# Performance work log

Hardware: AMD Instinct MI355X
Metric: run time of the kernel (lower is better)

Reference implementation:

```python
import jax, jax.numpy as jnp
import numpy as np

N = 50000; R2 = 200; D = 200; E = 200000; B = 1024
NB = 4; NF = 96; KS = 7; KW = 10; KH = 20
FLAT = (2 * KW - KS + 1) * (KH - KS + 1) * NF  # 18816
EPS = 1e-5


def _bn2d(x, g, b):
    # BatchNorm2d over NCHW with batch statistics
    m = x.mean(axis=(0, 2, 3), keepdims=True)
    v = x.var(axis=(0, 2, 3), keepdims=True)
    return (x - m) * jax.lax.rsqrt(v + EPS) * g[None, :, None, None] + b[None, :, None, None]


def _bn1d(x, g, b):
    m = x.mean(axis=0, keepdims=True)
    v = x.var(axis=0, keepdims=True)
    return (x - m) * jax.lax.rsqrt(v + EPS) * g[None, :] + b[None, :]


def setup_inputs() -> dict:
    key = jax.random.key(0)
    ks = jax.random.split(key, 16)
    s = 0.05
    return {
        'ent_emb': jax.random.normal(ks[0], (N, D)) * s,
        'rel_table': jax.random.normal(ks[1], (R2, D)) * s,
        'basis': jax.random.normal(ks[2], (NB, D, D)) * s,
        'att': jax.random.normal(ks[3], (R2, NB)) * s,
        'root': jax.random.normal(ks[4], (D, D)) * s,
        'gbias': jnp.zeros((D,), jnp.float32),
        'bn0_g': jnp.ones((1,), jnp.float32), 'bn0_b': jnp.zeros((1,), jnp.float32),
        'conv_k': jax.random.normal(ks[5], (NF, 1, KS, KS)) * s,
        'conv_b': jnp.zeros((NF,), jnp.float32),
        'bn1_g': jnp.ones((NF,), jnp.float32), 'bn1_b': jnp.zeros((NF,), jnp.float32),
        'fc_W': jax.random.normal(ks[6], (FLAT, D)) * s,
        'fc_b': jnp.zeros((D,), jnp.float32),
        'bn2_g': jnp.ones((D,), jnp.float32), 'bn2_b': jnp.zeros((D,), jnp.float32),
        'ent_bias': jnp.zeros((N,), jnp.float32),
        'edge_norm': jax.random.uniform(ks[7], (E,)),
        'entity': jnp.arange(N, dtype=jnp.int32),
        'edge_index': jax.random.randint(ks[8], (2, E), 0, N, dtype=jnp.int32),
        'edge_type': jax.random.randint(ks[9], (E,), 0, R2, dtype=jnp.int32),
        'src': jax.random.randint(ks[10], (B,), 0, N, dtype=jnp.int32),
        'rel': jax.random.randint(ks[11], (B,), 0, R2, dtype=jnp.int32),
    }


def reference(ent_emb, rel_table, basis, att, root, gbias, bn0_g, bn0_b,
              conv_k, conv_b, bn1_g, bn1_b, fc_W, fc_b, bn2_g, bn2_b,
              ent_bias, edge_norm, entity, edge_index, edge_type, src, rel):
    # --- MGCNConv: relational message passing ---
    x = ent_emb[entity]                                  # [N, D]
    xj = x[edge_index[0]]                                # gather source nodes [E, D]
    # basis-decomposed per-edge transform: msg_e = x_j @ (att[r_e] . basis)
    xb = jnp.einsum('ei,bio->ebo', xj, basis)            # [E, NB, D]
    msg = jnp.einsum('eb,ebo->eo', att[edge_type], xb)   # [E, D]
    msg = msg * edge_norm[:, None]
    aggr = jax.ops.segment_sum(msg, edge_index[1], num_segments=N)  # scatter-add [N, D]
    h = aggr + x @ root + gbias[None, :]                 # update (root + bias)

    # --- ConvE decoder ---
    src_e = h[src]                                       # [B, D]
    rel_e = rel_table[rel]                               # [B, D]
    stack = jnp.stack([src_e, rel_e], axis=1)            # [B, 2, D]
    xi = jnp.transpose(stack, (0, 2, 1)).reshape(-1, 1, 2 * KW, KH)  # [B,1,20,20]
    xi = _bn2d(xi, bn0_g, bn0_b)
    xi = jax.lax.conv_general_dilated(
        xi, conv_k, (1, 1), 'VALID',
        dimension_numbers=('NCHW', 'OIHW', 'NCHW')) + conv_b[None, :, None, None]
    xi = jax.nn.relu(_bn2d(xi, bn1_g, bn1_b))
    xi = xi.reshape(xi.shape[0], -1) @ fc_W + fc_b       # [B, D]
    xi = jax.nn.relu(_bn1d(xi, bn2_g, bn2_b))
    logits = xi @ h.T + ent_bias[None, :]                # [B, N]
    return jax.nn.sigmoid(logits)
```

## Files before the change

### kernel.cpp

```cpp
#include <hip/hip_runtime.h>
#include <hip/hip_bf16.h>

constexpr int N_ENT = 50000;
constexpr int D     = 200;
constexpr int NE    = 200000;
constexpr int BATCH = 1024;
constexpr int NF    = 96;
constexpr int FLAT  = 18816;
constexpr int KP    = 224;
constexpr float EPS = 1e-5f;

#define DEV static __device__ __forceinline__

typedef __attribute__((ext_vector_type(8))) __bf16 bf16x8;
typedef __attribute__((ext_vector_type(4))) float  f32x4;

DEV float bf2f(unsigned short u){ return __uint_as_float(((unsigned)u) << 16); }
DEV unsigned short f2bf(float f){
    unsigned u = __float_as_uint(f);
    return (unsigned short)((u + 0x7FFF + ((u >> 16) & 1)) >> 16);
}
DEV float sigmoidf(float x){ return 1.f / (1.f + __expf(-x)); }
DEV bf16x8 bzero8(){ bf16x8 v; 
    #pragma unroll
    for (int i = 0; i < 8; ++i) v[i] = (__bf16)0.f; 
    return v; }

__global__ __launch_bounds__(256) void k_pack_wb(const float* __restrict__ basis,
                                                 const float* __restrict__ root,
                                                 unsigned short* __restrict__ wb){
    int idx = blockIdx.x * 256 + threadIdx.x;
    if (idx >= 1008 * KP) return;
    int col = idx / KP, k = idx % KP;
    float v = 0.f;
    if (k < 200){
        if (col < 800){ int o = col >> 2, b = col & 3; v = basis[b * (D*D) + k * D + o]; }
        else if (col < 1000) v = root[k * D + (col - 800)];
    }
    wb[idx] = f2bf(v);
}

__global__ __launch_bounds__(256) void k_prep_eb(const float* __restrict__ ent_emb,
                                                 const int* __restrict__ entity,
                                                 unsigned short* __restrict__ eb){
    int gid = blockIdx.x * 256 + threadIdx.x;
    int m = gid / 28, k0 = (gid % 28) * 8;
    if (m >= 50048) return;
    unsigned short o[8];
    if (m < N_ENT){
        long base = (long)entity[m] * D;
        #pragma unroll
        for (int j = 0; j < 8; ++j){
            int k = k0 + j;
            o[j] = (k < D) ? f2bf(ent_emb[base + k]) : 0;
        }
    } else {
        #pragma unroll
        for (int j = 0; j < 8; ++j) o[j] = 0;
    }
    *(ushort4*)(eb + (long)m * KP + k0)     = make_ushort4(o[0], o[1], o[2], o[3]);
    *(ushort4*)(eb + (long)m * KP + k0 + 4) = make_ushort4(o[4], o[5], o[6], o[7]);
}

__global__ __launch_bounds__(256) void k_gemm_zh_mfma(const unsigned short* __restrict__ eb,
                                                      const unsigned short* __restrict__ wb,
                                                      const float* __restrict__ gbias,
                                                      unsigned short* __restrict__ z,
                                                      float* __restrict__ h){
    const int tid = threadIdx.x, w = tid >> 6, l = tid & 63;
    const int wm = w >> 1, wn = w & 1;
    const int m0 = blockIdx.y * 64 + wm * 32;
    const int n0 = blockIdx.x * 128 + wn * 64;
    const int lr = l & 15, lk = (l >> 4) * 8;
    f32x4 acc[2][4];
    #pragma unroll
    for (int mi = 0; mi < 2; ++mi)
        #pragma unroll
        for (int nj = 0; nj < 4; ++nj) acc[mi][nj] = (f32x4){0.f, 0.f, 0.f, 0.f};
    for (int k0 = 0; k0 < KP; k0 += 32){
        bf16x8 a[2], b[4];
        #pragma unroll
        for (int mi = 0; mi < 2; ++mi)
            a[mi] = *(const bf16x8*)(eb + (long)(m0 + mi*16 + lr) * KP + k0 + lk);
        #pragma unroll
        for (int nj = 0; nj < 4; ++nj){
            int col = n0 + nj*16 + lr;
            b[nj] = (col < 1008) ? *(const bf16x8*)(wb + (long)col * KP + k0 + lk) : bzero8();
        }
        #pragma unroll
        for (int mi = 0; mi < 2; ++mi)
            #pragma unroll
            for (int nj = 0; nj < 4; ++nj)
                acc[mi][nj] = __builtin_amdgcn_mfma_f32_16x16x32_bf16(a[mi], b[nj], acc[mi][nj], 0, 0, 0);
    }
    #pragma unroll
    for (int mi = 0; mi < 2; ++mi)
        #pragma unroll
        for (int r = 0; r < 4; ++r){
            int row = m0 + mi*16 + (l >> 4) * 4 + r;
            if (row >= N_ENT) continue;
            #pragma unroll
            for (int nj = 0; nj < 4; ++nj){
                int col = n0 + nj*16 + lr;
                float v = acc[mi][nj][r];
                if (col < 800)       z[(long)row * 800 + col] = f2bf(v);
                else if (col < 1000) h[row * D + (col - 800)] = v + gbias[col - 800];
            }
        }
}

__global__ __launch_bounds__(256) void k_edge(const unsigned short* __restrict__ z,
                                              float* __restrict__ h,
                                              const int* __restrict__ edge_index,
                                              const int* __restrict__ edge_type,
                                              const float* __restrict__ edge_norm,
                                              const float* __restrict__ att){
    int gtid = blockIdx.x * 256 + threadIdx.x;
    int wave = gtid >> 6, lane = gtid & 63;
    int nw = (gridDim.x * 256) >> 6;
    for (int e = wave; e < NE; e += nw){
        int src = edge_index[e];
        int dst = edge_index[NE + e];
        int r = edge_type[e];
        float nrm = edge_norm[e];
        float w0 = att[r*4+0]*nrm, w1 = att[r*4+1]*nrm, w2 = att[r*4+2]*nrm, w3 = att[r*4+3]*nrm;
        #pragma unroll
        for (int s = 0; s < 4; ++s){
            int d = lane + s * 64;
            if (d < D){
                ushort4 u = *(const ushort4*)(z + ((long)src * D + d) * 4);
                float v = w0*bf2f(u.x) + w1*bf2f(u.y) + w2*bf2f(u.z) + w3*bf2f(u.w);
                atomicAdd(h + dst * D + d, v);
            }
        }
    }
}

DEV void block_reduce2(float& s, float& ss, float* red){
    #pragma unroll
    for (int o = 32; o > 0; o >>= 1){ s += __shfl_down(s, o); ss += __shfl_down(ss, o); }
    int w = threadIdx.x >> 6;
    if ((threadIdx.x & 63) == 0){ red[w*2] = s; red[w*2+1] = ss; }
    __syncthreads();
    if (threadIdx.x == 0){
        #pragma unroll
        for (int i = 1; i < 4; ++i){ s += red[i*2]; ss += red[i*2+1]; }
    }
}

__global__ __launch_bounds__(256) void k_bn0_stats(const float* __restrict__ h,
                                                   const float* __restrict__ rel_table,
                                                   const int* __restrict__ srcb,
                                                   const int* __restrict__ relb,
                                                   float* __restrict__ stats){
    __shared__ float red[8];
    int b = blockIdx.x;
    int sb = srcb[b], rb = relb[b];
    float s = 0.f, ss = 0.f;
    for (int idx = threadIdx.x; idx < 2*D; idx += 256){
        float v = (idx < D) ? h[sb*D + idx] : rel_table[rb*D + (idx - D)];
        s += v; ss += v * v;
    }
    block_reduce2(s, ss, red);
    if (threadIdx.x == 0){ atomicAdd(&stats[0], s); atomicAdd(&stats[1], ss); }
}

__global__ __launch_bounds__(256) void k_h2bf(const float* __restrict__ h,
                                              unsigned short* __restrict__ hb){
    int gid = blockIdx.x * 256 + threadIdx.x;
    int m = gid / 28, k0 = (gid % 28) * 8;
    if (m >= 50048) return;
    unsigned short o[8];
    #pragma unroll
    for (int j = 0; j < 8; ++j){
        int k = k0 + j;
        o[j] = (m < N_ENT && k < D) ? f2bf(h[m*D + k]) : 0;
    }
    *(ushort4*)(hb + (long)m*KP + k0)     = make_ushort4(o[0], o[1], o[2], o[3]);
    *(ushort4*)(hb + (long)m*KP + k0 + 4) = make_ushort4(o[4], o[5], o[6], o[7]);
}

__global__ __launch_bounds__(256) void k_pack_fcw(const float* __restrict__ fc_W,
                                                  unsigned short* __restrict__ fcwt){
    __shared__ float t[32][33];
    int k0 = blockIdx.x * 32, n0 = blockIdx.y * 32;
    int tx = threadIdx.x & 31, ty = threadIdx.x >> 5;
    #pragma unroll
    for (int i = 0; i < 4; ++i){
        int k = k0 + ty + i*8, n = n0 + tx;
        t[ty + i*8][tx] = (n < D) ? fc_W[(long)k * D + n] : 0.f;
    }
    __syncthreads();
    #pragma unroll
    for (int i = 0; i < 4; ++i){
        int n = n0 + ty + i*8, k = k0 + tx;
        if (n < 208) fcwt[(long)n * FLAT + k] = f2bf(t[tx][ty + i*8]);
    }
}

__global__ __launch_bounds__(256) void k_pack_ckb(const float* __restrict__ conv_k,
                                                  const float* __restrict__ conv_b,
                                                  unsigned short* __restrict__ ckb){
    for (int idx = threadIdx.x; idx < NF * 64; idx += 256){
        int f = idx >> 6, k = idx & 63;
        float v = (k < 49) ? conv_k[f * 49 + k] : (k == 49 ? conv_b[f] : 0.f);
        ckb[idx] = f2bf(v);
    }
}

__global__ __launch_bounds__(256) void k_im2col(const float* __restrict__ h,
                                               const float* __restrict__ rel_table,
                                               const int* __restrict__ srcb,
                                               const int* __restrict__ relb,
                                               const float* __restrict__ stats,
                                               const float* __restrict__ bn0_g,
                                               const float* __restrict__ bn0_b,
                                               unsigned short* __restrict__ A){
    __shared__ float img[20][21];
    int b = blockIdx.x;
    float m0 = stats[0] * (1.f / 409600.f);
    float v0 = stats[1] * (1.f / 409600.f) - m0 * m0;
    float sc = rsqrtf(v0 + EPS) * bn0_g[0];
    float sh = bn0_b[0] - m0 * sc;
    int sb = srcb[b], rb = relb[b];
    for (int idx = threadIdx.x; idx < 400; idx += 256){
        int d = idx >> 1, c = idx & 1;
        float v = c ? rel_table[rb*D + d] : h[sb*D + d];
        img[idx / 20][idx % 20] = v * sc + sh;
    }
    __syncthreads();
    for (int idx = threadIdx.x; idx < 196 * 8; idx += 256){
        int p = idx >> 3, g = idx & 7;
        int oy = p / 14, ox = p % 14, k0 = g * 8;
        unsigned short o[8];
        #pragma unroll
        for (int j = 0; j < 8; ++j){
            int k = k0 + j;
            float v = 0.f;
            if (k < 49){ int ky = k / 7, kx = k % 7; v = img[oy + ky][ox + kx]; }
            else if (k == 49) v = 1.f;
            o[j] = f2bf(v);
        }
        long base = ((long)b * 196 + p) * 64 + k0;
        *(ushort4*)(A + base)     = make_ushort4(o[0], o[1], o[2], o[3]);
        *(ushort4*)(A + base + 4) = make_ushort4(o[4], o[5], o[6], o[7]);
    }
}

__global__ __launch_bounds__(256) void k_conv_mfma(const unsigned short* __restrict__ A,
                                                   const unsigned short* __restrict__ ckb,
                                                   unsigned short* __restrict__ conv_out){
    const int tid = threadIdx.x, w = tid >> 6, l = tid & 63;
    const int m0 = blockIdx.x * 128 + w * 32;
    const int lr = l & 15, lk = (l >> 4) * 8;
    f32x4 acc[2][6];
    #pragma unroll
    for (int mi = 0; mi < 2; ++mi)
        #pragma unroll
        for (int nj = 0; nj < 6; ++nj) acc[mi][nj] = (f32x4){0.f, 0.f, 0.f, 0.f};
    #pragma unroll
    for (int k0 = 0; k0 < 64; k0 += 32){
        bf16x8 a[2], b[6];
        #pragma unroll
        for (int mi = 0; mi < 2; ++mi)
            a[mi] = *(const bf16x8*)(A + (long)(m0 + mi*16 + lr) * 64 + k0 + lk);
        #pragma unroll
        for (int nj = 0; nj < 6; ++nj)
            b[nj] = *(const bf16x8*)(ckb + (nj*16 + lr) * 64 + k0 + lk);
        #pragma unroll
        for (int mi = 0; mi < 2; ++mi)
            #pragma unroll
            for (int nj = 0; nj < 6; ++nj)
                acc[mi][nj] = __builtin_amdgcn_mfma_f32_16x16x32_bf16(a[mi], b[nj], acc[mi][nj], 0, 0, 0);
    }
    #pragma unroll
    for (int mi = 0; mi < 2; ++mi)
        #pragma unroll
        for (int r = 0; r < 4; ++r){
            long row = m0 + mi*16 + (l >> 4) * 4 + r;
            #pragma unroll
            for (int nj = 0; nj < 6; ++nj)
                conv_out[row * 96 + nj*16 + lr] = f2bf(acc[mi][nj][r]);
        }
}

__global__ __launch_bounds__(256) void k_bn1_stats2(const unsigned short* __restrict__ conv_out,
                                                    float* __restrict__ s1sum,
                                                    float* __restrict__ s1ss){
    __shared__ float lsum[96], lss[96];
    int tid = threadIdx.x;
    if (tid < 96){ lsum[tid] = 0.f; lss[tid] = 0.f; }
    __syncthreads();
    if (tid < 192){
        int fg = tid % 24, rs = tid / 24;
        long r0 = (long)blockIdx.x * 784;
        float s[4] = {}, ss[4] = {};
        for (int i = 0; i < 98; ++i){
            long r = r0 + rs + i * 8;
            ushort4 u = *(const ushort4*)(conv_out + r * 96 + fg * 4);
            float v0 = bf2f(u.x), v1 = bf2f(u.y), v2 = bf2f(u.z), v3 = bf2f(u.w);
            s[0] += v0; ss[0] += v0*v0; s[1] += v1; ss[1] += v1*v1;
            s[2] += v2; ss[2] += v2*v2; s[3] += v3; ss[3] += v3*v3;
        }
        #pragma unroll
        for (int j = 0; j < 4; ++j){
            atomicAdd(&lsum[fg*4 + j], s[j]);
            atomicAdd(&lss[fg*4 + j], ss[j]);
        }
    }
    __syncthreads();
    if (tid < 96){
        atomicAdd(&s1sum[tid], lsum[tid]);
        atomicAdd(&s1ss[tid], lss[tid]);
    }
}

__global__ __launch_bounds__(128) void k_bn1_final(const float* __restrict__ s1sum,
                                                   const float* __restrict__ s1ss,
                                                   const float* __restrict__ bn1_g,
                                                   const float* __restrict__ bn1_b,
                                                   float* __restrict__ scale1,
                                                   float* __restrict__ shift1){
    int c = threadIdx.x;
    if (c < NF){
        float m = s1sum[c] * (1.f / 200704.f);
        float var = s1ss[c] * (1.f / 200704.f) - m * m;
        float scv = rsqrtf(var + EPS) * bn1_g[c];
        scale1[c] = scv;
        shift1[c] = bn1_b[c] - m * scv;
    }
}

__global__ __launch_bounds__(256) void k_bn1_tr(const unsigned short* __restrict__ conv_out,
                                                const float* __restrict__ scale1,
                                                const float* __restrict__ shift1,
                                                unsigned short* __restrict__ fcA){
    __shared__ unsigned short lds[FLAT];
    int b = blockIdx.x, tid = threadIdx.x;
    for (int idx = tid; idx < 2352; idx += 256){
        long base = (long)b * FLAT + idx * 8;
        ushort4 u0 = *(const ushort4*)(conv_out + base);
        ushort4 u1 = *(const ushort4*)(conv_out + base + 4);
        unsigned short in[8] = {u0.x,u0.y,u0.z,u0.w,u1.x,u1.y,u1.z,u1.w};
        unsigned short o[8];
        int f0 = (idx * 8) % 96;
        #pragma unroll
        for (int j = 0; j < 8; ++j){
            float v = bf2f(in[j]) * scale1[f0 + j] + shift1[f0 + j];
            o[j] = f2bf(fmaxf(v, 0.f));
        }
        *(ushort4*)(lds + idx*8)     = make_ushort4(o[0], o[1], o[2], o[3]);
        *(ushort4*)(lds + idx*8 + 4) = make_ushort4(o[4], o[5], o[6], o[7]);
    }
    __syncthreads();
    for (int idx = tid; idx < 4704; idx += 256){
        int q = idx * 4;
        int f = q / 196, p0 = q % 196;
        unsigned short o[4];
        #pragma unroll
        for (int j = 0; j < 4; ++j) o[j] = lds[(p0 + j) * 96 + f];
        *(ushort4*)(fcA + (long)b * FLAT + q) = make_ushort4(o[0], o[1], o[2], o[3]);
    }
}

__global__ __launch_bounds__(256) void k_fc_mfma(const unsigned short* __restrict__ ab,
                                                 const unsigned short* __restrict__ fcwt,
                                                 float* __restrict__ fc_out){
    const int tid = threadIdx.x, w = tid >> 6, l = tid & 63;
    const int wm = w >> 1, wn = w & 1;
    const int m0 = blockIdx.y * 64 + wm * 32;
    const int n0 = blockIdx.x * 64 + wn * 32;
    const int kb = blockIdx.z * 1568;
    const int lr = l & 15, lk = (l >> 4) * 8;
    f32x4 acc[2][2];
    #pragma unroll
    for (int mi = 0; mi < 2; ++mi)
        #pragma unroll
        for (int nj = 0; nj < 2; ++nj) acc[mi][nj] = (f32x4){0.f, 0.f, 0.f, 0.f};
    for (int k0 = kb; k0 < kb + 1568; k0 += 32){
        bf16x8 a[2], b[2];
        #pragma unroll
        for (int mi = 0; mi < 2; ++mi)
            a[mi] = *(const bf16x8*)(ab + (long)(m0 + mi*16 + lr) * FLAT + k0 + lk);
        #pragma unroll
        for (int nj = 0; nj < 2; ++nj){
            int col = n0 + nj*16 + lr;
            b[nj] = (col < 208) ? *(const bf16x8*)(fcwt + (long)col * FLAT + k0 + lk) : bzero8();
        }
        #pragma unroll
        for (int mi = 0; mi < 2; ++mi)
            #pragma unroll
            for (int nj = 0; nj < 2; ++nj)
                acc[mi][nj] = __builtin_amdgcn_mfma_f32_16x16x32_bf16(a[mi], b[nj], acc[mi][nj], 0, 0, 0);
    }
    #pragma unroll
    for (int mi = 0; mi < 2; ++mi)
        #pragma unroll
        for (int r = 0; r < 4; ++r){
            int row = m0 + mi*16 + (l >> 4) * 4 + r;
            #pragma unroll
            for (int nj = 0; nj < 2; ++nj){
                int col = n0 + nj*16 + lr;
                if (col < 208) atomicAdd(&fc_out[row * 208 + col], acc[mi][nj][r]);
            }
        }
}

__global__ __launch_bounds__(256) void k_bn2_stats(const float* __restrict__ fc_out,
                                                   const float* __restrict__ bn2_g,
                                                   const float* __restrict__ bn2_b,
                                                   float* __restrict__ sc2,
                                                   float* __restrict__ sh2){
    __shared__ float red[8];
    int n = blockIdx.x;
    float s = 0.f, ss = 0.f;
    for (int b = threadIdx.x; b < BATCH; b += 256){
        float v = fc_out[b * 208 + n];
        s += v; ss += v * v;
    }
    block_reduce2(s, ss, red);
    if (threadIdx.x == 0){
        float m = s * (1.f / 1024.f);
        float var = ss * (1.f / 1024.f) - m * m;
        float scv = rsqrtf(var + EPS) * bn2_g[n];
        sc2[n] = scv;
        sh2[n] = bn2_b[n] - m * scv;
    }
}

__global__ __launch_bounds__(256) void k_prep_logitsA(const float* __restrict__ fc_out,
                                                      const float* __restrict__ sc2,
                                                      const float* __restrict__ sh2,
                                                      unsigned short* __restrict__ ab_l){
    int idx = blockIdx.x * 256 + threadIdx.x;
    if (idx >= BATCH * KP) return;
    int b = idx / KP, k = idx % KP;
    float v = 0.f;
    if (k < D) v = fmaxf(fc_out[b * 208 + k] * sc2[k] + sh2[k], 0.f);
    ab_l[idx] = f2bf(v);
}

__global__ __launch_bounds__(256) void k_logits_mfma(const unsigned short* __restrict__ ab_l,
                                                     const unsigned short* __restrict__ hb,
                                                     const float* __restrict__ ent_bias,
                                                     float* __restrict__ out){
    const int tid = threadIdx.x, w = tid >> 6, l = tid & 63;
    const int wm = w >> 1, wn = w & 1;
    const int m0 = blockIdx.y * 64 + wm * 32;
    const int n0 = blockIdx.x * 128 + wn * 64;
    const int lr = l & 15, lk = (l >> 4) * 8;
    f32x4 acc[2][4];
    #pragma unroll
    for (int mi = 0; mi < 2; ++mi)
        #pragma unroll
        for (int nj = 0; nj < 4; ++nj) acc[mi][nj] = (f32x4){0.f, 0.f, 0.f, 0.f};
    for (int k0 = 0; k0 < KP; k0 += 32){
        bf16x8 a[2], b[4];
        #pragma unroll
        for (int mi = 0; mi < 2; ++mi)
            a[mi] = *(const bf16x8*)(ab_l + (long)(m0 + mi*16 + lr) * KP + k0 + lk);
        #pragma unroll
        for (int nj = 0; nj < 4; ++nj){
            int cb = n0 + nj*16;
            b[nj] = (cb < N_ENT) ? *(const bf16x8*)(hb + (long)(cb + lr) * KP + k0 + lk) : bzero8();
        }
        #pragma unroll
        for (int mi = 0; mi < 2; ++mi)
            #pragma unroll
            for (int nj = 0; nj < 4; ++nj)
                acc[mi][nj] = __builtin_amdgcn_mfma_f32_16x16x32_bf16(a[mi], b[nj], acc[mi][nj], 0, 0, 0);
    }
    #pragma unroll
    for (int mi = 0; mi < 2; ++mi)
        #pragma unroll
        for (int r = 0; r < 4; ++r){
            int row = m0 + mi*16 + (l >> 4) * 4 + r;
            #pragma unroll
            for (int nj = 0; nj < 4; ++nj){
                int cb = n0 + nj*16;
                if (cb < N_ENT){
                    int col = cb + lr;
                    out[(long)row * N_ENT + col] = sigmoidf(acc[mi][nj][r] + ent_bias[col]);
                }
            }
        }
}

extern "C" void kernel_launch(void* const* d_in, const int* in_sizes, int n_in,
                              void* d_out, int out_size, void* d_ws, size_t ws_size,
                              hipStream_t stream){
    const float* ent_emb   = (const float*)d_in[0];
    const float* rel_table = (const float*)d_in[1];
    const float* basis     = (const float*)d_in[2];
    const float* att       = (const float*)d_in[3];
    const float* root      = (const float*)d_in[4];
    const float* gbias     = (const float*)d_in[5];
    const float* bn0_g     = (const float*)d_in[6];
    const float* bn0_b     = (const float*)d_in[7];
    const float* conv_k    = (const float*)d_in[8];
    const float* conv_b    = (const float*)d_in[9];
    const float* bn1_g     = (const float*)d_in[10];
    const float* bn1_b     = (const float*)d_in[11];
    const float* fc_W      = (const float*)d_in[12];
    const float* bn2_g     = (const float*)d_in[14];
    const float* bn2_b     = (const float*)d_in[15];
    const float* ent_bias  = (const float*)d_in[16];
    const float* edge_norm = (const float*)d_in[17];
    const int*   entity    = (const int*)d_in[18];
    const int*   edge_index= (const int*)d_in[19];
    const int*   edge_type = (const int*)d_in[20];
    const int*   srcb      = (const int*)d_in[21];
    const int*   relb      = (const int*)d_in[22];
    float* out = (float*)d_out;

    char* ws = (char*)d_ws;
    unsigned short* z        = (unsigned short*)(ws);
    unsigned short* hb       = (unsigned short*)(ws);
    unsigned short* ckb      = (unsigned short*)(ws + 22500096);
    unsigned short* imA      = (unsigned short*)(ws + 24000000);
    unsigned short* fcA      = (unsigned short*)(ws + 24000000);
    unsigned short* fcwt     = (unsigned short*)(ws + 63000000);
    float*          h        = (float*)(ws + 80000000);
    unsigned short* conv_out = (unsigned short*)(ws + 120000000);
    unsigned short* eb       = (unsigned short*)(ws + 120000000);
    unsigned short* wb       = (unsigned short*)(ws + 158535168);
    float*          fc_out   = (float*)(ws + 158986752);
    unsigned short* ab_l     = (unsigned short*)(ws + 159838720);
    float*          stats    = (float*)(ws + 160297472);
    float* s1sum  = stats + 8;
    float* s1ss   = stats + 104;
    float* scale1 = stats + 200;
    float* shift1 = stats + 296;
    float* sc2    = stats + 392;
    float* sh2    = stats + 592;

    hipMemsetAsync(stats, 0, 4096, stream);
    hipMemsetAsync(fc_out, 0, BATCH * 208 * sizeof(float), stream);

    k_pack_wb      <<<(1008 * KP + 255) / 256, 256, 0, stream>>>(basis, root, wb);
    k_prep_eb      <<<(50048 * 28 + 255) / 256, 256, 0, stream>>>(ent_emb, entity, eb);
    k_gemm_zh_mfma <<<dim3(8, 782), 256, 0, stream>>>(eb, wb, gbias, z, h);
    k_edge         <<<2048, 256, 0, stream>>>(z, h, edge_index, edge_type, edge_norm, att);
    k_bn0_stats    <<<BATCH, 256, 0, stream>>>(h, rel_table, srcb, relb, stats);
    k_h2bf         <<<(50048 * 28 + 255) / 256, 256, 0, stream>>>(h, hb);
    k_pack_fcw     <<<dim3(588, 7), 256, 0, stream>>>(fc_W, fcwt);
    k_pack_ckb     <<<1, 256, 0, stream>>>(conv_k, conv_b, ckb);
    k_im2col       <<<BATCH, 256, 0, stream>>>(h, rel_table, srcb, relb, stats,
                                               bn0_g, bn0_b, imA);
    k_conv_mfma    <<<1568, 256, 0, stream>>>(imA, ckb, conv_out);
    k_bn1_stats2   <<<256, 256, 0, stream>>>(conv_out, s1sum, s1ss);
    k_bn1_final    <<<1, 128, 0, stream>>>(s1sum, s1ss, bn1_g, bn1_b, scale1, shift1);
    k_bn1_tr       <<<BATCH, 256, 0, stream>>>(conv_out, scale1, shift1, fcA);
    k_fc_mfma      <<<dim3(4, 16, 12), 256, 0, stream>>>(fcA, fcwt, fc_out);
    k_bn2_stats    <<<D, 256, 0, stream>>>(fc_out, bn2_g, bn2_b, sc2, sh2);
    k_prep_logitsA <<<(BATCH * KP + 255) / 256, 256, 0, stream>>>(fc_out, sc2, sh2, ab_l);
    k_logits_mfma  <<<dim3(391, 16), 256, 0, stream>>>(ab_l, hb, ent_bias, out);
}
```

Baseline: 893.8 us.

## Replace atomic edge scatter with CSR build and per-destination gather

Builds a CSR index of edges grouped by destination node (degree count, scan, fill) each call, then aggregates messages with one wave per destination accumulating in registers and a single write to h. This removes the per-element float atomicAdd traffic of the scatter kernel. In exchange it adds three small kernels, a memset and a single-block serial scan, and the floating-point summation order now depends on the atomic fill order.

```diff
diff --git a/kernel.cpp b/kernel.cpp
--- a/kernel.cpp
+++ b/kernel.cpp
@@ -109,30 +109,83 @@
         }
 }
 
-__global__ __launch_bounds__(256) void k_edge(const unsigned short* __restrict__ z,
-                                              float* __restrict__ h,
-                                              const int* __restrict__ edge_index,
-                                              const int* __restrict__ edge_type,
-                                              const float* __restrict__ edge_norm,
-                                              const float* __restrict__ att){
-    int gtid = blockIdx.x * 256 + threadIdx.x;
-    int wave = gtid >> 6, lane = gtid & 63;
-    int nw = (gridDim.x * 256) >> 6;
-    for (int e = wave; e < NE; e += nw){
+__global__ __launch_bounds__(256) void k_deg(const int* __restrict__ edge_index,
+                                             int* __restrict__ cnt){
+    int e = blockIdx.x * 256 + threadIdx.x;
+    if (e < NE) atomicAdd(&cnt[edge_index[NE + e]], 1);
+}
+
+__global__ __launch_bounds__(256) void k_scan(int* __restrict__ cnt,
+                                              int* __restrict__ rowptr){
+    __shared__ int sums[256];
+    const int t = threadIdx.x;
+    const int CH = 196;
+    int start = t * CH, end = min(start + CH, N_ENT);
+    int s = 0;
+    for (int i = start; i < end; ++i) s += cnt[i];
+    sums[t] = s;
+    __syncthreads();
+    if (t == 0){
+        int acc = 0;
+        for (int i = 0; i < 256; ++i){ int v = sums[i]; sums[i] = acc; acc += v; }
+        rowptr[N_ENT] = acc;
+    }
+    __syncthreads();
+    int acc = sums[t];
+    for (int i = start; i < end; ++i){
+        int v = cnt[i];
+        rowptr[i] = acc;
+        acc += v;
+        cnt[i] = 0;
+    }
+}
+
+__global__ __launch_bounds__(256) void k_fill(const int* __restrict__ edge_index,
+                                              const int* __restrict__ rowptr,
+                                              int* __restrict__ cnt,
+                                              int* __restrict__ eidx){
+    int e = blockIdx.x * 256 + threadIdx.x;
+    if (e >= NE) return;
+    int dst = edge_index[NE + e];
+    int pos = rowptr[dst] + atomicAdd(&cnt[dst], 1);
+    eidx[pos] = e;
+}
+
+__global__ __launch_bounds__(256) void k_edge_gather(const unsigned short* __restrict__ z,
+                                                     float* __restrict__ h,
+                                                     const int* __restrict__ edge_index,
+                                                     const int* __restrict__ edge_type,
+                                                     const float* __restrict__ edge_norm,
+                                                     const float* __restrict__ att,
+                                                     const int* __restrict__ rowptr,
+                                                     const int* __restrict__ eidx){
+    int gw = (blockIdx.x * 256 + threadIdx.x) >> 6;
+    int lane = threadIdx.x & 63;
+    if (gw >= N_ENT) return;
+    int beg = rowptr[gw], end = rowptr[gw + 1];
+    if (beg == end) return;
+    float acc[4] = {0.f, 0.f, 0.f, 0.f};
+    for (int i = beg; i < end; ++i){
+        int e = eidx[i];
         int src = edge_index[e];
-        int dst = edge_index[NE + e];
         int r = edge_type[e];
         float nrm = edge_norm[e];
-        float w0 = att[r*4+0]*nrm, w1 = att[r*4+1]*nrm, w2 = att[r*4+2]*nrm, w3 = att[r*4+3]*nrm;
+        float4 a = *(const float4*)(att + r * 4);
+        float w0 = a.x * nrm, w1 = a.y * nrm, w2 = a.z * nrm, w3 = a.w * nrm;
+        const unsigned short* zr = z + (long)src * 800;
         #pragma unroll
         for (int s = 0; s < 4; ++s){
             int d = lane + s * 64;
             if (d < D){
-                ushort4 u = *(const ushort4*)(z + ((long)src * D + d) * 4);
-                float v = w0*bf2f(u.x) + w1*bf2f(u.y) + w2*bf2f(u.z) + w3*bf2f(u.w);
-                atomicAdd(h + dst * D + d, v);
+                ushort4 u = *(const ushort4*)(zr + d * 4);
+                acc[s] += w0*bf2f(u.x) + w1*bf2f(u.y) + w2*bf2f(u.z) + w3*bf2f(u.w);
             }
         }
+    }
+    #pragma unroll
+    for (int s = 0; s < 4; ++s){
+        int d = lane + s * 64;
+        if (d < D) h[gw * D + d] += acc[s];
     }
 }
 
@@ -523,6 +576,9 @@
     float*          h        = (float*)(ws + 80000000);
     unsigned short* conv_out = (unsigned short*)(ws + 120000000);
     unsigned short* eb       = (unsigned short*)(ws + 120000000);
+    int*            rowptr   = (int*)(ws + 120000000);
+    int*            cntc     = (int*)(ws + 120200192);
+    int*            eidx     = (int*)(ws + 120400192);
     unsigned short* wb       = (unsigned short*)(ws + 158535168);
     float*          fc_out   = (float*)(ws + 158986752);
     unsigned short* ab_l     = (unsigned short*)(ws + 159838720);
@@ -540,7 +596,13 @@
     k_pack_wb      <<<(1008 * KP + 255) / 256, 256, 0, stream>>>(basis, root, wb);
     k_prep_eb      <<<(50048 * 28 + 255) / 256, 256, 0, stream>>>(ent_emb, entity, eb);
     k_gemm_zh_mfma <<<dim3(8, 782), 256, 0, stream>>>(eb, wb, gbias, z, h);
-    k_edge         <<<2048, 256, 0, stream>>>(z, h, edge_index, edge_type, edge_norm, att);
+    hipMemsetAsync(cntc, 0, N_ENT * sizeof(int), stream);
+    k_deg          <<<(NE + 255) / 256, 256, 0, stream>>>(edge_index, cntc);
+    k_scan         <<<1, 256, 0, stream>>>(cntc, rowptr);
+    k_fill         <<<(NE + 255) / 256, 256, 0, stream>>>(edge_index, rowptr, cntc, eidx);
+    k_edge_gather  <<<(N_ENT * 64 + 255) / 256, 256, 0, stream>>>(z, h, edge_index,
+                                                                  edge_type, edge_norm, att,
+                                                                  rowptr, eidx);
     k_bn0_stats    <<<BATCH, 256, 0, stream>>>(h, rel_table, srcb, relb, stats);
     k_h2bf         <<<(50048 * 28 + 255) / 256, 256, 0, stream>>>(h, hb);
     k_pack_fcw     <<<dim3(588, 7), 256, 0, stream>>>(fc_W, fcwt);
```

New measurement: 969.7 us. 1.08x slower.
